# Kernel optimization log

Hardware: AMD Instinct MI355X
Metric: run time of the kernel (lower is better)

Reference implementation:

```python
import jax, jax.numpy as jnp
import numpy as np
import math

S, W, H = 256, 128, 768   # sentence, word, hidden (hidden fixed to 768 by PositionalEncoding)
TOPK = 3                  # len(inputs) > 2 branch: fuse 3 nearest sentences


def positional_encoding(length, d_model):
    # Standard sinusoidal PE, identical to the torch buffer construction.
    pos = jnp.arange(length, dtype=jnp.float32)[:, None]                      # [L,1]
    div = jnp.exp(jnp.arange(0, d_model, 2, dtype=jnp.float32)
                  * (-math.log(10000.0) / d_model))                           # [H/2]
    pe = jnp.zeros((length, d_model), dtype=jnp.float32)
    pe = pe.at[:, 0::2].set(jnp.sin(pos * div))
    pe = pe.at[:, 1::2].set(jnp.cos(pos * div))
    return pe


def setup_inputs() -> dict:
    key = jax.random.key(0)
    inputs = jax.random.normal(key, (S, W, H), dtype=jnp.float32)
    return {"inputs": inputs}


def reference(inputs):
    s, w, h = inputs.shape
    # Pairwise L1 distance between the FIRST word vector of each sentence
    # (matmulCell only ever sees x[i,0,:] and k[0,j,:] == inputs[j,0,:]).
    x0 = inputs[:, 0, :]                                                      # [S,H]
    dist = jnp.sum(jnp.abs(x0[:, None, :] - x0[None, :, :]), axis=-1)         # [S,S]
    # torch.sort ascending -> 3 nearest sentences (self included, dist 0)
    idx = jnp.argsort(dist, axis=1)[:, :TOPK]                                 # [S,3] int
    fused = inputs[idx].reshape(s, TOPK * w, h)                               # [S,3W,H]
    # Positional encoding added to both q/v stream and k stream (same tensor;
    # dropout p=0.1 is identity in eval mode).
    x = fused + positional_encoding(TOPK * w, h)[None]                        # [S,3W,H]
    # Scaled dot-product self-attention per row.
    scores = jnp.einsum('slh,smh->slm', x, x) / jnp.sqrt(jnp.float32(h))      # [S,3W,3W]
    attn = jax.nn.softmax(scores, axis=-1)
    out = jnp.einsum('slm,smh->slh', attn, x)                                 # [S,3W,H]
    # D_Attention keeps only the first word-1 rows of each fused output.
    return out[:, :w - 1, :]                                                  # [S,W-1,H]
```

## Files before the change

### kernel.cpp

```cpp
#include <hip/hip_runtime.h>

#define NS 256
#define NW 128
#define NH 768
#define NL 384
#define WH (NW*NH)
#define OUTROWS 127

typedef __attribute__((ext_vector_type(8))) short short8;
typedef __attribute__((ext_vector_type(8))) unsigned short ushort8;
typedef __attribute__((ext_vector_type(8))) __bf16 bf16x8;
typedef __attribute__((ext_vector_type(4))) float f32x4;

#define XS_STRIDE 72
#define PS_STRIDE 392
#define SMEM_PS   (NL*XS_STRIDE*2)
#define SMEM_RED  (SMEM_PS + 128*PS_STRIDE*2)
#define SMEM_TOTAL (SMEM_RED + 4096)

__device__ __forceinline__ unsigned short bf16b(float f) {
  union { float f; unsigned u; } x; x.f = f;
  return (unsigned short)((x.u + 0x7fffu + ((x.u >> 16) & 1u)) >> 16);
}
__device__ __forceinline__ float b2f(unsigned short h) {
  union { unsigned u; float f; } x; x.u = ((unsigned)h) << 16;
  return x.f;
}
__device__ __forceinline__ unsigned short bfc(float f) {
  __bf16 h = (__bf16)f;
  return __builtin_bit_cast(unsigned short, h);
}

__global__ __launch_bounds__(1024) void k_pre(const float* __restrict__ inp,
                                              int* __restrict__ idxw,
                                              unsigned short* __restrict__ peb) {
  const int t = threadIdx.x;
  if (blockIdx.x >= NS) {
    int gid = (blockIdx.x - NS) * 1024 + t;
    if (gid < NL * NH) {
      int l = gid / NH, d = gid - l * NH;
      const float c = -0.011992630687355995f;
      float dv = __expf((float)(d & ~1) * c);
      float ang = (float)l * dv;
      float v = (d & 1) ? cosf(ang) : sinf(ang);
      peb[gid] = bf16b(v);
    }
    return;
  }
  const int i = blockIdx.x;
  __shared__ float xi[772];
  __shared__ float dist[NS];
  __shared__ unsigned long long wkeys[16];
  for (int h = t; h < NH; h += 1024) xi[h + h / 192] = inp[(size_t)i * WH + h];
  __syncthreads();
  const int c = t >> 2, seg = t & 3;
  const float* __restrict__ row = inp + (size_t)c * WH + seg * 192;
  const float* xis = xi + seg * 193;
  float s = 0.f;
  #pragma unroll 4
  for (int h = 0; h < 192; h += 4) {
    float4 v = *(const float4*)(row + h);
    s += fabsf(xis[h]     - v.x) + fabsf(xis[h + 1] - v.y)
       + fabsf(xis[h + 2] - v.z) + fabsf(xis[h + 3] - v.w);
  }
  s += __shfl_xor(s, 1, 64);
  s += __shfl_xor(s, 2, 64);
  if (seg == 0) dist[c] = s;
  __syncthreads();
  for (int k = 0; k < 3; ++k) {
    float d = (t < NS) ? dist[t] : 3.4e38f;
    unsigned long long key = ((unsigned long long)__float_as_uint(d) << 32) | (unsigned)t;
    #pragma unroll
    for (int dd = 1; dd < 64; dd <<= 1) {
      unsigned long long o = __shfl_xor(key, dd, 64);
      key = (o < key) ? o : key;
    }
    if ((t & 63) == 0) wkeys[t >> 6] = key;
    __syncthreads();
    if (t == 0) {
      unsigned long long best = wkeys[0];
      for (int w = 1; w < 16; ++w) if (wkeys[w] < best) best = wkeys[w];
      int bj = (int)(best & 0xffffffffu);
      idxw[i * 3 + k] = bj;
      dist[bj] = 3.4e38f;
    }
    __syncthreads();
  }
}

__global__ __launch_bounds__(512)
void k_attn(const float* __restrict__ inp, const unsigned short* __restrict__ peb,
            const int* __restrict__ idxw, float* __restrict__ out) {
  extern __shared__ char smem[];
  unsigned short* Xs = (unsigned short*)smem;
  unsigned short* Ps = (unsigned short*)(smem + SMEM_PS);
  float* red1 = (float*)(smem + SMEM_RED);
  float* red2 = red1 + 512;

  const int s = blockIdx.x;
  const int tid = threadIdx.x;
  const int lane = tid & 63, wid = tid >> 6;
  const int lrow = lane & 15, lhi = lane >> 4;
  const int i0 = idxw[s * 3 + 0], i1 = idxw[s * 3 + 1], i2 = idxw[s * 3 + 2];

  const f32x4 fz = {0.f, 0.f, 0.f, 0.f};
  f32x4 acc[4][6];
  #pragma unroll
  for (int qs = 0; qs < 4; ++qs)
    #pragma unroll
    for (int kf = 0; kf < 6; ++kf) acc[qs][kf] = fz;

  const int qh = wid & 1, kq = wid >> 1;
  const int rl0 = tid >> 3, c8 = (tid & 7) * 8;

  for (int hc = 0; hc < 12; ++hc) {
    const int h0 = hc * 64;
    #pragma unroll
    for (int it = 0; it < 6; ++it) {
      const int src = (it < 2) ? i0 : (it < 4 ? i1 : i2);
      const int rl = rl0 + (it & 1) * 64;
      const int r  = rl + (it >> 1) * 128;
      const float* px = inp + (size_t)src * WH + (size_t)rl * NH + h0 + c8;
      float4 a = *(const float4*)px;
      float4 b = *(const float4*)(px + 4);
      ushort8 pv = *(const ushort8*)&peb[r * NH + h0 + c8];
      bf16x8 o;
      o[0] = (__bf16)(a.x + b2f(pv[0])); o[1] = (__bf16)(a.y + b2f(pv[1]));
      o[2] = (__bf16)(a.z + b2f(pv[2])); o[3] = (__bf16)(a.w + b2f(pv[3]));
      o[4] = (__bf16)(b.x + b2f(pv[4])); o[5] = (__bf16)(b.y + b2f(pv[5]));
      o[6] = (__bf16)(b.z + b2f(pv[6])); o[7] = (__bf16)(b.w + b2f(pv[7]));
      *reinterpret_cast<bf16x8*>(&Xs[r * XS_STRIDE + c8]) = o;
    }
    __syncthreads();
    __builtin_amdgcn_s_setprio(1);
    #pragma unroll
    for (int ks = 0; ks < 64; ks += 32) {
      short8 a[4];
      #pragma unroll
      for (int qs = 0; qs < 4; ++qs)
        a[qs] = *reinterpret_cast<const short8*>(&Xs[(qh * 64 + qs * 16 + lrow) * XS_STRIDE + ks + lhi * 8]);
      #pragma unroll
      for (int kf = 0; kf < 6; ++kf) {
        short8 b = *reinterpret_cast<const short8*>(&Xs[(kq * 96 + kf * 16 + lrow) * XS_STRIDE + ks + lhi * 8]);
        #pragma unroll
        for (int qs = 0; qs < 4; ++qs)
          acc[qs][kf] = __builtin_amdgcn_mfma_f32_16x16x32_bf16(a[qs], b, acc[qs][kf], 0, 0, 0);
      }
    }
    __builtin_amdgcn_s_setprio(0);
    __syncthreads();
  }

  const float scale = 0.03608439182435161f;
  float mx[4][4];
  #pragma unroll
  for (int qs = 0; qs < 4; ++qs)
    #pragma unroll
    for (int r = 0; r < 4; ++r) {
      float m = acc[qs][0][r];
      #pragma unroll
      for (int kf = 1; kf < 6; ++kf) m = fmaxf(m, acc[qs][kf][r]);
      #pragma unroll
      for (int d = 1; d < 16; d <<= 1) m = fmaxf(m, __shfl_xor(m, d, 64));
      mx[qs][r] = m;
    }
  if (lrow == 0) {
    #pragma unroll
    for (int qs = 0; qs < 4; ++qs)
      #pragma unroll
      for (int r = 0; r < 4; ++r)
        red1[(qh * 64 + qs * 16 + lhi * 4 + r) * 4 + kq] = mx[qs][r];
  }
  __syncthreads();
  float sm[4][4];
  #pragma unroll
  for (int qs = 0; qs < 4; ++qs)
    #pragma unroll
    for (int r = 0; r < 4; ++r) {
      const int row = qh * 64 + qs * 16 + lhi * 4 + r;
      float4 m0 = *(const float4*)&red1[row * 4];
      mx[qs][r] = fmaxf(fmaxf(m0.x, m0.y), fmaxf(m0.z, m0.w));
      sm[qs][r] = 0.f;
    }
  #pragma unroll
  for (int qs = 0; qs < 4; ++qs)
    #pragma unroll
    for (int kf = 0; kf < 6; ++kf)
      #pragma unroll
      for (int r = 0; r < 4; ++r) {
        float p = __expf((acc[qs][kf][r] - mx[qs][r]) * scale);
        acc[qs][kf][r] = p;
        sm[qs][r] += p;
      }
  #pragma unroll
  for (int qs = 0; qs < 4; ++qs)
    #pragma unroll
    for (int r = 0; r < 4; ++r) {
      #pragma unroll
      for (int d = 1; d < 16; d <<= 1) sm[qs][r] += __shfl_xor(sm[qs][r], d, 64);
    }
  if (lrow == 0) {
    #pragma unroll
    for (int qs = 0; qs < 4; ++qs)
      #pragma unroll
      for (int r = 0; r < 4; ++r)
        red2[(qh * 64 + qs * 16 + lhi * 4 + r) * 4 + kq] = sm[qs][r];
  }
  __syncthreads();
  #pragma unroll
  for (int qs = 0; qs < 4; ++qs)
    #pragma unroll
    for (int r = 0; r < 4; ++r) {
      const int row = qh * 64 + qs * 16 + lhi * 4 + r;
      float4 s0 = *(const float4*)&red2[row * 4];
      sm[qs][r] = 1.0f / ((s0.x + s0.y) + (s0.z + s0.w));
    }
  #pragma unroll
  for (int qs = 0; qs < 4; ++qs)
    #pragma unroll
    for (int kf = 0; kf < 6; ++kf)
      #pragma unroll
      for (int r = 0; r < 4; ++r) {
        const int row = qh * 64 + qs * 16 + lhi * 4 + r;
        const int col = kq * 96 + kf * 16 + lrow;
        *(unsigned short*)((char*)Ps + (((row * PS_STRIDE + col) * 2) ^ (((row >> 3) & 7) << 4))) =
            bfc(acc[qs][kf][r] * sm[qs][r]);
      }
  __syncthreads();

  const int qb = wid & 3, hh = wid >> 2;
  short8 pa[2][12];
  #pragma unroll
  for (int qs = 0; qs < 2; ++qs)
    #pragma unroll
    for (int m0 = 0; m0 < 12; ++m0) {
      const int row = qb * 32 + qs * 16 + lrow;
      pa[qs][m0] = *reinterpret_cast<const short8*>(
          (const char*)Ps + (((row * PS_STRIDE + m0 * 32 + lhi * 8) * 2) ^ (((row >> 3) & 7) << 4)));
    }

  unsigned short* VT = Xs;
  for (int t4 = 0; t4 < 12; ++t4) {
    const int h0 = t4 * 64;
    #pragma unroll
    for (int it = 0; it < 6; ++it) {
      const int src = (it < 2) ? i0 : (it < 4 ? i1 : i2);
      const int ml = rl0 + (it & 1) * 64;
      const int m  = ml + (it >> 1) * 128;
      const float* px = inp + (size_t)src * WH + (size_t)ml * NH + h0 + c8;
      float4 a = *(const float4*)px;
      float4 b = *(const float4*)(px + 4);
      ushort8 pv = *(const ushort8*)&peb[m * NH + h0 + c8];
      float v[8];
      v[0] = a.x + b2f(pv[0]); v[1] = a.y + b2f(pv[1]);
      v[2] = a.z + b2f(pv[2]); v[3] = a.w + b2f(pv[3]);
      v[4] = b.x + b2f(pv[4]); v[5] = b.y + b2f(pv[5]);
      v[6] = b.z + b2f(pv[6]); v[7] = b.w + b2f(pv[7]);
      #pragma unroll
      for (int j = 0; j < 8; ++j) {
        const int vr = c8 + j;
        VT[((vr * PS_STRIDE) + m) ^ (((vr >> 3) & 7) << 3)] = bfc(v[j]);
      }
    }
    __syncthreads();
    __builtin_amdgcn_s_setprio(1);
    f32x4 o00 = fz, o01 = fz, o10 = fz, o11 = fz;
    const int vr0 = hh * 32 + lrow, vr1 = vr0 + 16;
    const int sw0 = ((vr0 >> 3) & 7) << 4, sw1 = ((vr1 >> 3) & 7) << 4;
    #pragma unroll
    for (int mm = 0; mm < 12; ++mm) {
      const int moff = (mm * 32 + lhi * 8) * 2;
      short8 b0 = *reinterpret_cast<const short8*>((const char*)VT + ((vr0 * PS_STRIDE * 2 + moff) ^ sw0));
      short8 b1 = *reinterpret_cast<const short8*>((const char*)VT + ((vr1 * PS_STRIDE * 2 + moff) ^ sw1));
      o00 = __builtin_amdgcn_mfma_f32_16x16x32_bf16(pa[0][mm], b0, o00, 0, 0, 0);
      o01 = __builtin_amdgcn_mfma_f32_16x16x32_bf16(pa[0][mm], b1, o01, 0, 0, 0);
      o10 = __builtin_amdgcn_mfma_f32_16x16x32_bf16(pa[1][mm], b0, o10, 0, 0, 0);
      o11 = __builtin_amdgcn_mfma_f32_16x16x32_bf16(pa[1][mm], b1, o11, 0, 0, 0);
    }
    __builtin_amdgcn_s_setprio(0);
    float* ob = out + (size_t)s * (OUTROWS * NH) + h0 + hh * 32 + lrow;
    #pragma unroll
    for (int qs = 0; qs < 2; ++qs)
      #pragma unroll
      for (int hf = 0; hf < 2; ++hf) {
        f32x4 o = (qs == 0) ? (hf == 0 ? o00 : o01) : (hf == 0 ? o10 : o11);
        #pragma unroll
        for (int r = 0; r < 4; ++r) {
          const int q = qb * 32 + qs * 16 + lhi * 4 + r;
          if (q < OUTROWS) ob[(size_t)q * NH + hf * 16] = o[r];
        }
      }
    __syncthreads();
  }
}

extern "C" void kernel_launch(void* const* d_in, const int* in_sizes, int n_in,
                              void* d_out, int out_size, void* d_ws, size_t ws_size,
                              hipStream_t stream) {
  (void)in_sizes; (void)n_in; (void)out_size; (void)ws_size;
  const float* inp = (const float*)d_in[0];
  float* out = (float*)d_out;
  char* ws = (char*)d_ws;

  unsigned short* peb = (unsigned short*)ws;
  int* idxw           = (int*)(ws + 589824);

  hipLaunchKernelGGL(k_pre, dim3(256 + 288), dim3(1024), 0, stream, inp, idxw, peb);

  hipFuncSetAttribute((const void*)k_attn,
                      hipFuncAttributeMaxDynamicSharedMemorySize, SMEM_TOTAL);
  hipLaunchKernelGGL(k_attn, dim3(256), dim3(512), SMEM_TOTAL, stream,
                     inp, peb, idxw, out);
}
```

Before: 136.1 us.

## Pre-convert input to bf16 and widen QK^T hidden chunk to 128

Adds a pass in the prep kernel that converts the entire fp32 input to a bf16 copy in workspace. The attention kernel then reads bf16 for both the QK^T and PV staging, which halves the bytes it gathers. The QK^T loop now stages 128 hidden columns per step instead of 64, so there are half as many barriers. In exchange, every call must read the full fp32 input and write a bf16 copy, and rounding x before adding the positional encoding adds a second rounding step.

New measurement: 127.7 us. -6.1%, faster.

```diff
diff --git a/kernel.cpp b/kernel.cpp
--- a/kernel.cpp
+++ b/kernel.cpp
@@ -12,9 +12,9 @@
 typedef __attribute__((ext_vector_type(8))) __bf16 bf16x8;
 typedef __attribute__((ext_vector_type(4))) float f32x4;
 
-#define XS_STRIDE 72
+#define XS2_STRIDE 136
 #define PS_STRIDE 392
-#define SMEM_PS   (NL*XS_STRIDE*2)
+#define SMEM_PS   55296
 #define SMEM_RED  (SMEM_PS + 128*PS_STRIDE*2)
 #define SMEM_TOTAL (SMEM_RED + 4096)
 
@@ -33,21 +33,31 @@
 
 __global__ __launch_bounds__(1024) void k_pre(const float* __restrict__ inp,
                                               int* __restrict__ idxw,
-                                              unsigned short* __restrict__ peb) {
+                                              unsigned short* __restrict__ peb,
+                                              unsigned short* __restrict__ inpb) {
   const int t = threadIdx.x;
-  if (blockIdx.x >= NS) {
-    int gid = (blockIdx.x - NS) * 1024 + t;
-    if (gid < NL * NH) {
-      int l = gid / NH, d = gid - l * NH;
-      const float c = -0.011992630687355995f;
-      float dv = __expf((float)(d & ~1) * c);
-      float ang = (float)l * dv;
-      float v = (d & 1) ? cosf(ang) : sinf(ang);
-      peb[gid] = bf16b(v);
-    }
+  const int b = blockIdx.x;
+  if (b >= 544) {
+    size_t base = ((size_t)(b - 544) * 1024 + t) * 8;
+    float4 a = *(const float4*)(inp + base);
+    float4 c = *(const float4*)(inp + base + 4);
+    ushort8 o;
+    o[0] = bfc(a.x); o[1] = bfc(a.y); o[2] = bfc(a.z); o[3] = bfc(a.w);
+    o[4] = bfc(c.x); o[5] = bfc(c.y); o[6] = bfc(c.z); o[7] = bfc(c.w);
+    *(ushort8*)(inpb + base) = o;
     return;
   }
-  const int i = blockIdx.x;
+  if (b >= NS) {
+    int gid = (b - NS) * 1024 + t;
+    int l = gid / NH, d = gid - l * NH;
+    const float c = -0.011992630687355995f;
+    float dv = __expf((float)(d & ~1) * c);
+    float ang = (float)l * dv;
+    float v = (d & 1) ? cosf(ang) : sinf(ang);
+    peb[gid] = bf16b(v);
+    return;
+  }
+  const int i = b;
   __shared__ float xi[772];
   __shared__ float dist[NS];
   __shared__ unsigned long long wkeys[16];
@@ -89,7 +99,7 @@
 }
 
 __global__ __launch_bounds__(512)
-void k_attn(const float* __restrict__ inp, const unsigned short* __restrict__ peb,
+void k_attn(const unsigned short* __restrict__ inpb, const unsigned short* __restrict__ peb,
             const int* __restrict__ idxw, float* __restrict__ out) {
   extern __shared__ char smem[];
   unsigned short* Xs = (unsigned short*)smem;
@@ -111,37 +121,33 @@
     for (int kf = 0; kf < 6; ++kf) acc[qs][kf] = fz;
 
   const int qh = wid & 1, kq = wid >> 1;
-  const int rl0 = tid >> 3, c8 = (tid & 7) * 8;
-
-  for (int hc = 0; hc < 12; ++hc) {
-    const int h0 = hc * 64;
-    #pragma unroll
-    for (int it = 0; it < 6; ++it) {
-      const int src = (it < 2) ? i0 : (it < 4 ? i1 : i2);
-      const int rl = rl0 + (it & 1) * 64;
-      const int r  = rl + (it >> 1) * 128;
-      const float* px = inp + (size_t)src * WH + (size_t)rl * NH + h0 + c8;
-      float4 a = *(const float4*)px;
-      float4 b = *(const float4*)(px + 4);
-      ushort8 pv = *(const ushort8*)&peb[r * NH + h0 + c8];
+
+  for (int hc = 0; hc < 6; ++hc) {
+    const int h0 = hc * 128;
+    #pragma unroll
+    for (int it = 0; it < 12; ++it) {
+      const int src = (it < 4) ? i0 : (it < 8 ? i1 : i2);
+      const int rls = (it & 3) * 32 + (tid >> 4);
+      const int r   = it * 32 + (tid >> 4);
+      const int cc  = (tid & 15) * 8;
+      ushort8 xv = *(const ushort8*)&inpb[(size_t)src * WH + (size_t)rls * NH + h0 + cc];
+      ushort8 pv = *(const ushort8*)&peb[r * NH + h0 + cc];
       bf16x8 o;
-      o[0] = (__bf16)(a.x + b2f(pv[0])); o[1] = (__bf16)(a.y + b2f(pv[1]));
-      o[2] = (__bf16)(a.z + b2f(pv[2])); o[3] = (__bf16)(a.w + b2f(pv[3]));
-      o[4] = (__bf16)(b.x + b2f(pv[4])); o[5] = (__bf16)(b.y + b2f(pv[5]));
-      o[6] = (__bf16)(b.z + b2f(pv[6])); o[7] = (__bf16)(b.w + b2f(pv[7]));
-      *reinterpret_cast<bf16x8*>(&Xs[r * XS_STRIDE + c8]) = o;
+      #pragma unroll
+      for (int j = 0; j < 8; ++j) o[j] = (__bf16)(b2f(xv[j]) + b2f(pv[j]));
+      *reinterpret_cast<bf16x8*>(&Xs[r * XS2_STRIDE + cc]) = o;
     }
     __syncthreads();
     __builtin_amdgcn_s_setprio(1);
     #pragma unroll
-    for (int ks = 0; ks < 64; ks += 32) {
+    for (int ks = 0; ks < 128; ks += 32) {
       short8 a[4];
       #pragma unroll
       for (int qs = 0; qs < 4; ++qs)
-        a[qs] = *reinterpret_cast<const short8*>(&Xs[(qh * 64 + qs * 16 + lrow) * XS_STRIDE + ks + lhi * 8]);
+        a[qs] = *reinterpret_cast<const short8*>(&Xs[(qh * 64 + qs * 16 + lrow) * XS2_STRIDE + ks + lhi * 8]);
       #pragma unroll
       for (int kf = 0; kf < 6; ++kf) {
-        short8 b = *reinterpret_cast<const short8*>(&Xs[(kq * 96 + kf * 16 + lrow) * XS_STRIDE + ks + lhi * 8]);
+        short8 b = *reinterpret_cast<const short8*>(&Xs[(kq * 96 + kf * 16 + lrow) * XS2_STRIDE + ks + lhi * 8]);
         #pragma unroll
         for (int qs = 0; qs < 4; ++qs)
           acc[qs][kf] = __builtin_amdgcn_mfma_f32_16x16x32_bf16(a[qs], b, acc[qs][kf], 0, 0, 0);
@@ -240,6 +246,7 @@
     }
 
   unsigned short* VT = Xs;
+  const int rl0 = tid >> 3, c8 = (tid & 7) * 8;
   for (int t4 = 0; t4 < 12; ++t4) {
     const int h0 = t4 * 64;
     #pragma unroll
@@ -247,19 +254,12 @@
       const int src = (it < 2) ? i0 : (it < 4 ? i1 : i2);
       const int ml = rl0 + (it & 1) * 64;
       const int m  = ml + (it >> 1) * 128;
-      const float* px = inp + (size_t)src * WH + (size_t)ml * NH + h0 + c8;
-      float4 a = *(const float4*)px;
-      float4 b = *(const float4*)(px + 4);
+      ushort8 xv = *(const ushort8*)&inpb[(size_t)src * WH + (size_t)ml * NH + h0 + c8];
       ushort8 pv = *(const ushort8*)&peb[m * NH + h0 + c8];
-      float v[8];
-      v[0] = a.x + b2f(pv[0]); v[1] = a.y + b2f(pv[1]);
-      v[2] = a.z + b2f(pv[2]); v[3] = a.w + b2f(pv[3]);
-      v[4] = b.x + b2f(pv[4]); v[5] = b.y + b2f(pv[5]);
-      v[6] = b.z + b2f(pv[6]); v[7] = b.w + b2f(pv[7]);
       #pragma unroll
       for (int j = 0; j < 8; ++j) {
         const int vr = c8 + j;
-        VT[((vr * PS_STRIDE) + m) ^ (((vr >> 3) & 7) << 3)] = bfc(v[j]);
+        VT[((vr * PS_STRIDE) + m) ^ (((vr >> 3) & 7) << 3)] = bfc(b2f(xv[j]) + b2f(pv[j]));
       }
     }
     __syncthreads();
@@ -304,11 +304,13 @@
 
   unsigned short* peb = (unsigned short*)ws;
   int* idxw           = (int*)(ws + 589824);
-
-  hipLaunchKernelGGL(k_pre, dim3(256 + 288), dim3(1024), 0, stream, inp, idxw, peb);
+  unsigned short* inpb= (unsigned short*)(ws + 592896);
+
+  hipLaunchKernelGGL(k_pre, dim3(256 + 288 + 3072), dim3(1024), 0, stream,
+                     inp, idxw, peb, inpb);
 
   hipFuncSetAttribute((const void*)k_attn,
                       hipFuncAttributeMaxDynamicSharedMemorySize, SMEM_TOTAL);
   hipLaunchKernelGGL(k_attn, dim3(256), dim3(512), SMEM_TOTAL, stream,
-                     inp, peb, idxw, out);
-}
+                     inpb, peb, idxw, out);
+}
```
